# Kernel optimization log

Hardware: AMD Instinct MI355X
Metric: run time of the kernel (lower is better)

Reference implementation:

```python
import math
import jax, jax.numpy as jnp
import numpy as np

NUM_BUCKETS = 32
MAX_DISTANCE = 128
N_HEADS = 16
D_KV = 64


def relative_position_bucket(rel_pos, num_buckets=NUM_BUCKETS, max_distance=MAX_DISTANCE):
    # bidirectional=True path of the original
    n = -rel_pos
    nb = num_buckets // 2
    ret = (n < 0).astype(jnp.int32) * nb
    n = jnp.abs(n)
    max_exact = nb // 2
    is_small = n < max_exact
    val_large = max_exact + (
        jnp.log(n.astype(jnp.float32) / max_exact)
        / math.log(max_distance / max_exact)
        * (nb - max_exact)
    ).astype(jnp.int32)
    val_large = jnp.minimum(val_large, nb - 1)
    return jnp.where(is_small, n, val_large) + ret


def setup_inputs() -> dict:
    key = jax.random.key(0)
    ks = jax.random.split(key, 6)
    B, S, D = 2, 2048, 1024
    inner = N_HEADS * D_KV  # 1024
    sc = 1.0 / math.sqrt(D)
    return {
        "x": jax.random.normal(ks[0], (B, S, D), dtype=jnp.float32),
        "Wq": jax.random.normal(ks[1], (D, inner), dtype=jnp.float32) * sc,
        "Wk": jax.random.normal(ks[2], (D, inner), dtype=jnp.float32) * sc,
        "Wv": jax.random.normal(ks[3], (D, inner), dtype=jnp.float32) * sc,
        "Wo": jax.random.normal(ks[4], (inner, D), dtype=jnp.float32) * sc,
        "rel_table": jax.random.normal(ks[5], (NUM_BUCKETS, N_HEADS), dtype=jnp.float32),
        "attention_mask": jnp.zeros((B, 1, 1, S), dtype=jnp.float32),
    }


def reference(x, Wq, Wk, Wv, Wo, rel_table, attention_mask):
    B, S, D = x.shape
    H, Dk = N_HEADS, D_KV

    q = (x @ Wq).reshape(B, S, H, Dk).transpose(0, 2, 1, 3)  # bhqd
    k = (x @ Wk).reshape(B, S, H, Dk).transpose(0, 2, 1, 3)
    v = (x @ Wv).reshape(B, S, H, Dk).transpose(0, 2, 1, 3)

    # NOTE: T5 attention has no 1/sqrt(d) scaling
    scores = jnp.einsum('bhqd,bhkd->bhqk', q.astype(jnp.float32), k.astype(jnp.float32))

    pos = jnp.arange(S)
    rel_pos = pos[None, :] - pos[:, None]  # [S,S] = k_pos - q_pos
    buckets = relative_position_bucket(rel_pos)
    position_bias = jnp.transpose(rel_table[buckets], (2, 0, 1))  # [H,S,S]

    scores = scores + position_bias[None, ...] + attention_mask
    weights = jax.nn.softmax(scores, axis=-1)
    out = jnp.einsum('bhqk,bhkd->bhqd', weights, v.astype(jnp.float32))
    out = out.transpose(0, 2, 1, 3).reshape(B, S, H * Dk).astype(x.dtype)
    out = out @ Wo
    return (out, position_bias)
```

## Files before the change

### kernel.cpp

```cpp
#include <hip/hip_runtime.h>
#include <hip/hip_bf16.h>
#include <math.h>
#include <stdint.h>

typedef __bf16 bf16_t;
typedef __attribute__((ext_vector_type(8))) __bf16 bf16x8;
typedef __attribute__((ext_vector_type(4))) float f32x4;
typedef float f32x4a __attribute__((ext_vector_type(4), aligned(4)));
typedef unsigned short u16;
typedef unsigned int u32;

#define DEV static __device__ __forceinline__
#define LOG2E 1.4426950408889634f

DEV u16 f2b(float f){ bf16_t h = (bf16_t)f; return __builtin_bit_cast(u16, h); }
DEV float b2f(u16 u){ bf16_t h = __builtin_bit_cast(bf16_t, u); return (float)h; }
DEV f32x4 mfma16(bf16x8 a, bf16x8 b, f32x4 c){
  return __builtin_amdgcn_mfma_f32_16x16x32_bf16(a, b, c, 0, 0, 0);
}

#if __has_builtin(__builtin_amdgcn_exp2f)
DEV float fexp2(float x){ return __builtin_amdgcn_exp2f(x); }
#else
DEV float fexp2(float x){ return exp2f(x); }
#endif

DEV void gld16(const void* g, void* l){
  __builtin_amdgcn_global_load_lds((const __attribute__((address_space(1))) u32*)g,
                                   (__attribute__((address_space(3))) u32*)l, 16, 0, 0);
}

DEV bf16x8 ldsA64(const u16* arr, int row, int ch){
  return *(const bf16x8*)&arr[row*64 + ((ch ^ (row&7))*8)];
}
DEV bf16x8 ldsA32(const u16* arr, int row, int ch){
  return *(const bf16x8*)&arr[row*32 + ((ch ^ ((row>>1)&3))*8)];
}

__global__ __launch_bounds__(256) void k_prep(const float* __restrict__ x,
                                              const float* __restrict__ Wq, const float* __restrict__ Wk,
                                              const float* __restrict__ Wv, const float* __restrict__ Wo,
                                              const float* __restrict__ rel_table, const float* __restrict__ mask,
                                              u16* __restrict__ xh, u16* __restrict__ xl,
                                              u16* __restrict__ wth, u16* __restrict__ wot,
                                              float* __restrict__ bt, float* __restrict__ bt2,
                                              float* __restrict__ msk2){
  __shared__ float tile[64][65];
  int bid = blockIdx.x;
  int t = threadIdx.x;
  if(bid < 4096){
    size_t i = ((size_t)bid*256 + t)*4;
    float4 v = *(const float4*)(x + i);
    ushort4 hv, lv; float f, hf;
    f=v.x; hv.x=f2b(f); hf=b2f(hv.x); lv.x=f2b(f-hf);
    f=v.y; hv.y=f2b(f); hf=b2f(hv.y); lv.y=f2b(f-hf);
    f=v.z; hv.z=f2b(f); hf=b2f(hv.z); lv.z=f2b(f-hf);
    f=v.w; hv.w=f2b(f); hf=b2f(hv.w); lv.w=f2b(f-hf);
    *(ushort4*)(xh+i) = hv;
    *(ushort4*)(xl+i) = lv;
  } else if(bid < 5120){
    int rr = bid - 4096;
    int z = rr >> 8, ky = (rr >> 4) & 15, nx = rr & 15;
    const float* W = (z==0)?Wq:((z==1)?Wk:((z==2)?Wv:Wo));
    int n0 = nx*64, k0 = ky*64;
    int r = t>>6, c = t&63;
    #pragma unroll
    for(int i=0;i<16;i++){
      int row = i*4 + r;
      tile[row][c] = W[(size_t)(k0+row)*1024 + n0 + c];
    }
    __syncthreads();
    #pragma unroll
    for(int i=0;i<16;i++){
      int nrow = i*4 + r;
      float v = tile[c][nrow];
      size_t o = (size_t)(n0+nrow)*1024 + k0 + c;
      if(z<3) wth[(size_t)z*1048576 + o] = f2b(v);
      else    wot[o] = f2b(v);
    }
  } else {
    int gid = (bid-5120)*256 + t;
    if(gid < 4096) msk2[gid] = mask[gid]*LOG2E;
    int h = gid >> 12, idx = gid & 4095;
    float v = 0.f;
    if(idx < 4095){
      int delta = idx - 2047;
      int n = -delta;
      int ret = 0;
      if(n < 0){ ret = 16; n = -n; }
      int bucket;
      if(n < 8) bucket = n + ret;
      else {
        float a = (float)log((double)n * 0.125);
        float rr2 = (float)((double)a / (double)2.7725887298583984f);
        int vl = 8 + (int)(rr2 * 8.0f);
        vl = vl > 15 ? 15 : vl;
        bucket = vl + ret;
      }
      v = rel_table[bucket*16 + h];
    }
    bt[gid] = v;
    bt2[gid] = v*LOG2E - 32.0f;
  }
}

__global__ __launch_bounds__(256) void k_gemm_qkv(const u16* __restrict__ xh, const u16* __restrict__ xl,
                                                  const u16* __restrict__ wth,
                                                  u16* __restrict__ qh, u16* __restrict__ ql,
                                                  u16* __restrict__ kh, u16* __restrict__ vt){
  __shared__ __align__(16) u16 SM[17408];
  u16* Ah = SM; u16* Al = SM+4096; u16* Bh = SM+8192;
  int z = blockIdx.z;
  const u16* WH = wth + (size_t)z*1048576;
  int m0 = blockIdx.y*128, n0 = blockIdx.x*128;
  int t = threadIdx.x, w = t>>6, lane = t&63, l16 = lane&15, g = lane>>4;
  f32x4 acc[4][4];
  #pragma unroll
  for(int i=0;i<4;i++)
    #pragma unroll
    for(int j=0;j<4;j++) acc[i][j] = {0.f,0.f,0.f,0.f};
  int rbase = (w>>1)*64, cbase = (w&1)*64;
  for(int k0=0;k0<1024;k0+=32){
    __syncthreads();
    #pragma unroll
    for(int jj=0;jj<6;jj++){
      int q = w + 4*jj;
      int arr = q>>3, sub = q&7;
      if(z!=0 && arr==1) continue;
      int row = sub*16 + (lane>>2);
      int lch = (lane&3) ^ ((row>>1)&3);
      const u16* src;
      if(arr==0)      src = xh + (size_t)(m0+row)*1024 + k0 + lch*8;
      else if(arr==1) src = xl + (size_t)(m0+row)*1024 + k0 + lch*8;
      else            src = WH + (size_t)(n0+row)*1024 + k0 + lch*8;
      gld16(src, &SM[q*512]);
    }
    __syncthreads();
    if(z!=0){
      bf16x8 ah[4];
      #pragma unroll
      for(int i=0;i<4;i++) ah[i] = ldsA32(Ah, rbase + i*16 + l16, g);
      #pragma unroll
      for(int j=0;j<4;j++){
        bf16x8 bh = ldsA32(Bh, cbase + j*16 + l16, g);
        #pragma unroll
        for(int i=0;i<4;i++)
          acc[i][j] = mfma16(ah[i], bh, acc[i][j]);
      }
    } else {
      bf16x8 ah[4], am[4];
      #pragma unroll
      for(int i=0;i<4;i++){
        int row = rbase + i*16 + l16;
        ah[i] = ldsA32(Ah, row, g);
        am[i] = ldsA32(Al, row, g);
      }
      #pragma unroll
      for(int j=0;j<4;j++){
        bf16x8 bh = ldsA32(Bh, cbase + j*16 + l16, g);
        #pragma unroll
        for(int i=0;i<4;i++){
          acc[i][j] = mfma16(ah[i], bh, acc[i][j]);
          acc[i][j] = mfma16(am[i], bh, acc[i][j]);
        }
      }
    }
  }
  if(z==2){
    __syncthreads();
    #pragma unroll
    for(int i=0;i<4;i++)
      #pragma unroll
      for(int j=0;j<4;j++)
        #pragma unroll
        for(int r=0;r<4;r++){
          int ml = rbase + i*16 + g*4 + r;
          int nl = cbase + j*16 + l16;
          SM[nl*136 + ml] = f2b(acc[i][j][r]);
        }
    __syncthreads();
    int bb = m0 >> 11;
    #pragma unroll
    for(int kk=0;kk<8;kk++){
      int id = t + 256*kk;
      int row = id>>4, ch = id&15;
      uint4 v = *(const uint4*)&SM[row*136 + ch*8];
      int n = n0 + row;
      size_t dst = ((size_t)(bb*16 + (n>>6))*64 + (n&63))*2048 + (m0&2047) + ch*8;
      *(uint4*)&vt[dst] = v;
    }
  } else {
    #pragma unroll
    for(int i=0;i<4;i++)
      #pragma unroll
      for(int j=0;j<4;j++)
        #pragma unroll
        for(int r=0;r<4;r++){
          int m = m0 + rbase + i*16 + g*4 + r;
          int n = n0 + cbase + j*16 + l16;
          float v = acc[i][j][r];
          if(z==0) v *= LOG2E;
          int b = m >> 11, s = m & 2047;
          int hh = n >> 6, d = n & 63;
          size_t a = ((size_t)(b*16+hh)*2048 + s)*64 + d;
          u16 hb = f2b(v);
          if(z==0){ qh[a]=hb; ql[a]=f2b(v - b2f(hb)); }
          else    { kh[a]=hb; }
        }
  }
}

__global__ __launch_bounds__(256) void k_attn(const u16* __restrict__ qh, const u16* __restrict__ ql,
                                              const u16* __restrict__ kh,
                                              const u16* __restrict__ vt, const float* __restrict__ bt2,
                                              const float* __restrict__ msk2,
                                              const float* __restrict__ bt, float* __restrict__ bias_out,
                                              u16* __restrict__ ao){
  __shared__ __align__(16) u16 SM[12800];
  u16* KH = SM; u16* VT = SM+4096;
  int bh = blockIdx.y, b = bh>>4, h = bh&15;
  int q0 = blockIdx.x*64;
  int t = threadIdx.x, w = t>>6, lane = t&63, l16 = lane&15, g = lane>>4;
  size_t base  = (size_t)bh*2048*64;
  size_t vbase = (size_t)bh*64*2048;
  u16* PSw = SM + 8192 + w*1152;
  const float* bt2h = bt2 + h*4096;
  const float* msk2b = msk2 + b*2048;
  size_t wbase = ((size_t)(bh*32 + blockIdx.x))*65536 + t*8;

  bf16x8 qfh[2], qfl[2];
  {
    int qr = q0 + w*16 + l16;
    size_t a0 = base + (size_t)qr*64 + g*8;
    qfh[0] = *(const bf16x8*)&qh[a0];
    qfl[0] = *(const bf16x8*)&ql[a0];
    qfh[1] = *(const bf16x8*)&qh[a0+32];
    qfl[1] = *(const bf16x8*)&ql[a0+32];
  }
  f32x4 O[4];
  float rs[4];
  #pragma unroll
  for(int jd=0;jd<4;jd++) O[jd] = {0.f,0.f,0.f,0.f};
  #pragma unroll
  for(int r=0;r<4;r++) rs[r] = 0.f;
  int qgbase = q0 + w*16 + g*4;

  for(int k0=0;k0<2048;k0+=64){
    __syncthreads();
    #pragma unroll
    for(int jj=0;jj<4;jj++){
      int q = w + 4*jj;
      int arr = q>>3, sub = q&7;
      int row = sub*8 + (lane>>3);
      int lch = (lane&7) ^ (row&7);
      const u16* src;
      if(arr==0) src = kh + base + (size_t)(k0+row)*64 + lch*8;
      else       src = vt + vbase + (size_t)row*2048 + k0 + lch*8;
      gld16(src, &SM[q*512]);
    }
    {
      size_t f = wbase + (size_t)(k0>>6)*2048;
      int hh = (int)(f >> 22);
      int rem = (int)(f & 4194303);
      int qq = rem >> 11;
      int kk = rem & 2047;
      const float* row = bt + hh*4096 + (kk - qq + 2047);
      f32x4a v0 = *(const f32x4a*)(row);
      f32x4a v1 = *(const f32x4a*)(row + 4);
      *(f32x4a*)(bias_out + f)     = v0;
      *(f32x4a*)(bias_out + f + 4) = v1;
    }
    f32x4 sc[4];
    {
      const float* bb = bt2h + (k0 + l16 + 2047 - qgbase);
      #pragma unroll
      for(int j=0;j<4;j++){
        f32x4a ld = *(const f32x4a*)(bb + j*16 - 3);
        float mk = msk2b[k0 + j*16 + l16];
        sc[j] = (f32x4){ld[3]+mk, ld[2]+mk, ld[1]+mk, ld[0]+mk};
      }
    }
    __syncthreads();
    #pragma unroll
    for(int j=0;j<4;j++){
      int krow = j*16 + l16;
      bf16x8 kfh0 = ldsA64(KH, krow, g);
      bf16x8 kfh1 = ldsA64(KH, krow, 4+g);
      f32x4 s = sc[j];
      s = mfma16(qfh[0], kfh0, s);
      s = mfma16(qfl[0], kfh0, s);
      s = mfma16(qfh[1], kfh1, s);
      s = mfma16(qfl[1], kfh1, s);
      sc[j] = s;
    }
    #pragma unroll
    for(int j=0;j<4;j++){
      #pragma unroll
      for(int r=0;r<4;r++){
        float p = fexp2(sc[j][r]);
        rs[r] += p;
        PSw[(g*4+r)*72 + j*16 + l16] = f2b(p);
      }
    }
    #pragma unroll
    for(int ds=0; ds<2; ds++){
      bf16x8 pa = *(const bf16x8*)&PSw[l16*72 + ds*32 + g*8];
      #pragma unroll
      for(int jd=0;jd<4;jd++){
        bf16x8 vb = ldsA64(VT, jd*16 + l16, ds*4 + g);
        O[jd] = mfma16(pa, vb, O[jd]);
      }
    }
  }
  #pragma unroll
  for(int r=0;r<4;r++){
    float v = rs[r];
    v += __shfl_xor(v,1,64);
    v += __shfl_xor(v,2,64);
    v += __shfl_xor(v,4,64);
    v += __shfl_xor(v,8,64);
    float inv = 1.f/v;
    int q = qgbase + r;
    size_t a = ((size_t)(b*2048 + q))*1024 + h*64;
    #pragma unroll
    for(int jd=0;jd<4;jd++)
      ao[a + jd*16 + l16] = f2b(O[jd][r]*inv);
  }
}

__global__ __launch_bounds__(256) void k_gemm_out(const u16* __restrict__ ao, const u16* __restrict__ wot,
                                                  float* __restrict__ out){
  __shared__ __align__(16) u16 SM[8192];
  u16* As = SM; u16* Bs = SM+4096;
  int m0 = blockIdx.y*128, n0 = blockIdx.x*128;
  int t = threadIdx.x, w = t>>6, lane = t&63, l16 = lane&15, g = lane>>4;
  f32x4 acc[4][4];
  #pragma unroll
  for(int i=0;i<4;i++)
    #pragma unroll
    for(int j=0;j<4;j++) acc[i][j] = {0.f,0.f,0.f,0.f};
  int rbase = (w>>1)*64, cbase = (w&1)*64;
  for(int k0=0;k0<1024;k0+=32){
    __syncthreads();
    #pragma unroll
    for(int jj=0;jj<4;jj++){
      int q = w + 4*jj;
      int arr = q>>3, sub = q&7;
      int row = sub*16 + (lane>>2);
      int lch = (lane&3) ^ ((row>>1)&3);
      const u16* src;
      if(arr==0) src = ao  + (size_t)(m0+row)*1024 + k0 + lch*8;
      else       src = wot + (size_t)(n0+row)*1024 + k0 + lch*8;
      gld16(src, &SM[q*512]);
    }
    __syncthreads();
    bf16x8 af[4];
    #pragma unroll
    for(int i=0;i<4;i++) af[i] = ldsA32(As, rbase + i*16 + l16, g);
    #pragma unroll
    for(int j=0;j<4;j++){
      bf16x8 bfb = ldsA32(Bs, cbase + j*16 + l16, g);
      #pragma unroll
      for(int i=0;i<4;i++)
        acc[i][j] = mfma16(af[i], bfb, acc[i][j]);
    }
  }
  #pragma unroll
  for(int i=0;i<4;i++)
    #pragma unroll
    for(int j=0;j<4;j++)
      #pragma unroll
      for(int r=0;r<4;r++){
        int m = m0 + rbase + i*16 + g*4 + r;
        int n = n0 + cbase + j*16 + l16;
        out[(size_t)m*1024 + n] = acc[i][j][r];
      }
}

extern "C" void kernel_launch(void* const* d_in, const int* in_sizes, int n_in,
                              void* d_out, int out_size, void* d_ws, size_t ws_size,
                              hipStream_t stream) {
  const float* x   = (const float*)d_in[0];
  const float* Wq  = (const float*)d_in[1];
  const float* Wk  = (const float*)d_in[2];
  const float* Wv  = (const float*)d_in[3];
  const float* Wo  = (const float*)d_in[4];
  const float* rel = (const float*)d_in[5];
  const float* msk = (const float*)d_in[6];
  float* out = (float*)d_out;
  float* bias_out = out + (size_t)4194304;
  char* ws = (char*)d_ws;
  u16* xh  = (u16*)(ws + 0);
  u16* xl  = (u16*)(ws + 8388608);
  u16* wth = (u16*)(ws + 16777216);
  u16* wot = (u16*)(ws + 23068672);
  u16* qh  = (u16*)(ws + 25165824);
  u16* ql  = (u16*)(ws + 33554432);
  u16* kh  = (u16*)(ws + 41943040);
  u16* vt  = (u16*)(ws + 50331648);
  u16* ao  = (u16*)(ws + 58720256);
  float* bt  = (float*)(ws + 67108864);
  float* bt2 = (float*)(ws + 67371008);
  float* msk2= (float*)(ws + 67633152);

  k_prep      <<<5376, 256, 0, stream>>>(x, Wq, Wk, Wv, Wo, rel, msk,
                                         xh, xl, wth, wot, bt, bt2, msk2);
  k_gemm_qkv  <<<dim3(8,32,3), 256, 0, stream>>>(xh, xl, wth, qh, ql, kh, vt);
  k_attn      <<<dim3(32,32), 256, 0, stream>>>(qh, ql, kh, vt, bt2, msk2, bt, bias_out, ao);
  k_gemm_out  <<<dim3(8,32), 256, 0, stream>>>(ao, wot, out);
}
```

Baseline: 487.1 us.

## Double-buffer K/V tiles and process 128 queries per attention block

The attention kernel now handles 128 query rows per block (two 16-row groups per wave), so each K/V tile loaded into LDS is reused across twice as many queries. It also double-buffers the K/V tiles in LDS, issuing the next tile's loads before computing on the current one, which cuts the barriers per iteration from two to one. The position-bias copy is widened to match the larger tile. In exchange, registers and LDS per block roughly double and the grid halves to 512 blocks, which may reduce occupancy and latency hiding.

```diff
diff --git a/kernel.cpp b/kernel.cpp
--- a/kernel.cpp
+++ b/kernel.cpp
@@ -210,56 +210,92 @@
   }
 }
 
-__global__ __launch_bounds__(256) void k_attn(const u16* __restrict__ qh, const u16* __restrict__ ql,
+__global__ __launch_bounds__(256,2) void k_attn(const u16* __restrict__ qh, const u16* __restrict__ ql,
                                               const u16* __restrict__ kh,
                                               const u16* __restrict__ vt, const float* __restrict__ bt2,
                                               const float* __restrict__ msk2,
                                               const float* __restrict__ bt, float* __restrict__ bias_out,
                                               u16* __restrict__ ao){
-  __shared__ __align__(16) u16 SM[12800];
-  u16* KH = SM; u16* VT = SM+4096;
+  __shared__ __align__(16) u16 SM[25600];
   int bh = blockIdx.y, b = bh>>4, h = bh&15;
-  int q0 = blockIdx.x*64;
+  int q0 = blockIdx.x*128;
   int t = threadIdx.x, w = t>>6, lane = t&63, l16 = lane&15, g = lane>>4;
   size_t base  = (size_t)bh*2048*64;
   size_t vbase = (size_t)bh*64*2048;
-  u16* PSw = SM + 8192 + w*1152;
+  u16* PSw = SM + 16384 + w*2304;
   const float* bt2h = bt2 + h*4096;
   const float* msk2b = msk2 + b*2048;
-  size_t wbase = ((size_t)(bh*32 + blockIdx.x))*65536 + t*8;
-
-  bf16x8 qfh[2], qfl[2];
-  {
-    int qr = q0 + w*16 + l16;
+  size_t wbase = ((size_t)(bh*16 + blockIdx.x))*131072 + t*16;
+
+  bf16x8 qfh[2][2], qfl[2][2];
+  int qgb0 = q0 + w*32 + g*4;
+  #pragma unroll
+  for(int qg=0; qg<2; qg++){
+    int qr = q0 + w*32 + qg*16 + l16;
     size_t a0 = base + (size_t)qr*64 + g*8;
-    qfh[0] = *(const bf16x8*)&qh[a0];
-    qfl[0] = *(const bf16x8*)&ql[a0];
-    qfh[1] = *(const bf16x8*)&qh[a0+32];
-    qfl[1] = *(const bf16x8*)&ql[a0+32];
-  }
-  f32x4 O[4];
-  float rs[4];
-  #pragma unroll
-  for(int jd=0;jd<4;jd++) O[jd] = {0.f,0.f,0.f,0.f};
-  #pragma unroll
-  for(int r=0;r<4;r++) rs[r] = 0.f;
-  int qgbase = q0 + w*16 + g*4;
-
-  for(int k0=0;k0<2048;k0+=64){
-    __syncthreads();
-    #pragma unroll
-    for(int jj=0;jj<4;jj++){
-      int q = w + 4*jj;
-      int arr = q>>3, sub = q&7;
-      int row = sub*8 + (lane>>3);
-      int lch = (lane&7) ^ (row&7);
-      const u16* src;
-      if(arr==0) src = kh + base + (size_t)(k0+row)*64 + lch*8;
-      else       src = vt + vbase + (size_t)row*2048 + k0 + lch*8;
-      gld16(src, &SM[q*512]);
-    }
+    qfh[qg][0] = *(const bf16x8*)&qh[a0];
+    qfl[qg][0] = *(const bf16x8*)&ql[a0];
+    qfh[qg][1] = *(const bf16x8*)&qh[a0+32];
+    qfl[qg][1] = *(const bf16x8*)&ql[a0+32];
+  }
+  f32x4 O[2][4];
+  float rs[2][4];
+  #pragma unroll
+  for(int qg=0;qg<2;qg++){
+    #pragma unroll
+    for(int jd=0;jd<4;jd++) O[qg][jd] = {0.f,0.f,0.f,0.f};
+    #pragma unroll
+    for(int r=0;r<4;r++) rs[qg][r] = 0.f;
+  }
+
+  #pragma unroll
+  for(int jj=0;jj<4;jj++){
+    int q = w + 4*jj;
+    int arr = q>>3, sub = q&7;
+    int row = sub*8 + (lane>>3);
+    int lch = (lane&7) ^ (row&7);
+    const u16* src = (arr==0) ? kh + base + (size_t)row*64 + lch*8
+                              : vt + vbase + (size_t)row*2048 + lch*8;
+    gld16(src, &SM[q*512]);
+  }
+  __syncthreads();
+
+  for(int it=0; it<32; it++){
+    int k0 = it*64;
+    int cur = it & 1;
+    const u16* KH = SM + cur*8192;
+    const u16* VT = KH + 4096;
+    f32x4 sc[2][4];
     {
-      size_t f = wbase + (size_t)(k0>>6)*2048;
+      float mk[4];
+      #pragma unroll
+      for(int j=0;j<4;j++) mk[j] = msk2b[k0 + j*16 + l16];
+      #pragma unroll
+      for(int qg=0;qg<2;qg++){
+        const float* bb = bt2h + (k0 + l16 + 2047 - (qgb0 + qg*16));
+        #pragma unroll
+        for(int j=0;j<4;j++){
+          f32x4a ld = *(const f32x4a*)(bb + j*16 - 3);
+          sc[qg][j] = (f32x4){ld[3]+mk[j], ld[2]+mk[j], ld[1]+mk[j], ld[0]+mk[j]};
+        }
+      }
+    }
+    if(it < 31){
+      u16* dst = SM + (cur^1)*8192;
+      int kn = k0 + 64;
+      #pragma unroll
+      for(int jj=0;jj<4;jj++){
+        int q = w + 4*jj;
+        int arr = q>>3, sub = q&7;
+        int row = sub*8 + (lane>>3);
+        int lch = (lane&7) ^ (row&7);
+        const u16* src = (arr==0) ? kh + base + (size_t)(kn+row)*64 + lch*8
+                                  : vt + vbase + (size_t)row*2048 + kn + lch*8;
+        gld16(src, dst + q*512);
+      }
+    }
+    {
+      size_t f = wbase + (size_t)it*4096;
       int hh = (int)(f >> 22);
       int rem = (int)(f & 4194303);
       int qq = rem >> 11;
@@ -267,65 +303,67 @@
       const float* row = bt + hh*4096 + (kk - qq + 2047);
       f32x4a v0 = *(const f32x4a*)(row);
       f32x4a v1 = *(const f32x4a*)(row + 4);
-      *(f32x4a*)(bias_out + f)     = v0;
-      *(f32x4a*)(bias_out + f + 4) = v1;
-    }
-    f32x4 sc[4];
-    {
-      const float* bb = bt2h + (k0 + l16 + 2047 - qgbase);
-      #pragma unroll
-      for(int j=0;j<4;j++){
-        f32x4a ld = *(const f32x4a*)(bb + j*16 - 3);
-        float mk = msk2b[k0 + j*16 + l16];
-        sc[j] = (f32x4){ld[3]+mk, ld[2]+mk, ld[1]+mk, ld[0]+mk};
-      }
-    }
-    __syncthreads();
+      f32x4a v2 = *(const f32x4a*)(row + 8);
+      f32x4a v3 = *(const f32x4a*)(row + 12);
+      *(f32x4a*)(bias_out + f)      = v0;
+      *(f32x4a*)(bias_out + f + 4)  = v1;
+      *(f32x4a*)(bias_out + f + 8)  = v2;
+      *(f32x4a*)(bias_out + f + 12) = v3;
+    }
     #pragma unroll
     for(int j=0;j<4;j++){
       int krow = j*16 + l16;
-      bf16x8 kfh0 = ldsA64(KH, krow, g);
-      bf16x8 kfh1 = ldsA64(KH, krow, 4+g);
-      f32x4 s = sc[j];
-      s = mfma16(qfh[0], kfh0, s);
-      s = mfma16(qfl[0], kfh0, s);
-      s = mfma16(qfh[1], kfh1, s);
-      s = mfma16(qfl[1], kfh1, s);
-      sc[j] = s;
-    }
-    #pragma unroll
-    for(int j=0;j<4;j++){
-      #pragma unroll
-      for(int r=0;r<4;r++){
-        float p = fexp2(sc[j][r]);
-        rs[r] += p;
-        PSw[(g*4+r)*72 + j*16 + l16] = f2b(p);
-      }
-    }
+      bf16x8 kf0 = ldsA64(KH, krow, g);
+      bf16x8 kf1 = ldsA64(KH, krow, 4+g);
+      #pragma unroll
+      for(int qg=0;qg<2;qg++){
+        f32x4 s = sc[qg][j];
+        s = mfma16(qfh[qg][0], kf0, s);
+        s = mfma16(qfl[qg][0], kf0, s);
+        s = mfma16(qfh[qg][1], kf1, s);
+        s = mfma16(qfl[qg][1], kf1, s);
+        sc[qg][j] = s;
+      }
+    }
+    #pragma unroll
+    for(int qg=0;qg<2;qg++)
+      #pragma unroll
+      for(int j=0;j<4;j++)
+        #pragma unroll
+        for(int r=0;r<4;r++){
+          float p = fexp2(sc[qg][j][r]);
+          rs[qg][r] += p;
+          PSw[(qg*16 + g*4 + r)*72 + j*16 + l16] = f2b(p);
+        }
     #pragma unroll
     for(int ds=0; ds<2; ds++){
-      bf16x8 pa = *(const bf16x8*)&PSw[l16*72 + ds*32 + g*8];
+      bf16x8 pa0 = *(const bf16x8*)&PSw[l16*72 + ds*32 + g*8];
+      bf16x8 pa1 = *(const bf16x8*)&PSw[(16 + l16)*72 + ds*32 + g*8];
       #pragma unroll
       for(int jd=0;jd<4;jd++){
         bf16x8 vb = ldsA64(VT, jd*16 + l16, ds*4 + g);
-        O[jd] = mfma16(pa, vb, O[jd]);
-      }
-    }
-  }
-  #pragma unroll
-  for(int r=0;r<4;r++){
-    float v = rs[r];
-    v += __shfl_xor(v,1,64);
-    v += __shfl_xor(v,2,64);
-    v += __shfl_xor(v,4,64);
-    v += __shfl_xor(v,8,64);
-    float inv = 1.f/v;
-    int q = qgbase + r;
-    size_t a = ((size_t)(b*2048 + q))*1024 + h*64;
-    #pragma unroll
-    for(int jd=0;jd<4;jd++)
-      ao[a + jd*16 + l16] = f2b(O[jd][r]*inv);
-  }
+        O[0][jd] = mfma16(pa0, vb, O[0][jd]);
+        O[1][jd] = mfma16(pa1, vb, O[1][jd]);
+      }
+    }
+    __syncthreads();
+  }
+  #pragma unroll
+  for(int qg=0;qg<2;qg++)
+    #pragma unroll
+    for(int r=0;r<4;r++){
+      float v = rs[qg][r];
+      v += __shfl_xor(v,1,64);
+      v += __shfl_xor(v,2,64);
+      v += __shfl_xor(v,4,64);
+      v += __shfl_xor(v,8,64);
+      float inv = 1.f/v;
+      int q = qgb0 + qg*16 + r;
+      size_t a = ((size_t)(b*2048 + q))*1024 + h*64;
+      #pragma unroll
+      for(int jd=0;jd<4;jd++)
+        ao[a + jd*16 + l16] = f2b(O[qg][jd][r]*inv);
+    }
 }
 
 __global__ __launch_bounds__(256) void k_gemm_out(const u16* __restrict__ ao, const u16* __restrict__ wot,
@@ -406,6 +444,6 @@
   k_prep      <<<5376, 256, 0, stream>>>(x, Wq, Wk, Wv, Wo, rel, msk,
                                          xh, xl, wth, wot, bt, bt2, msk2);
   k_gemm_qkv  <<<dim3(8,32,3), 256, 0, stream>>>(xh, xl, wth, qh, ql, kh, vt);
-  k_attn      <<<dim3(32,32), 256, 0, stream>>>(qh, ql, kh, vt, bt2, msk2, bt, bias_out, ao);
+  k_attn      <<<dim3(16,32), 256, 0, stream>>>(qh, ql, kh, vt, bt2, msk2, bt, bias_out, ao);
   k_gemm_out  <<<dim3(8,32), 256, 0, stream>>>(ao, wot, out);
 }
```

Measured after the change: 514.0 us. 1.06x slower.
